# Optimization experiments

Hardware: AMD Instinct MI355X
Metric: run time of the kernel (lower is better)

## Reference

```python
import jax, jax.numpy as jnp
import numpy as np

H = 16  # num_heads

def setup_inputs() -> dict:
    key = jax.random.key(0)
    k1, k2, k3, k4 = jax.random.split(key, 4)
    B, N, E = 2, 2048, 2048
    return {
        "hidden_states": jax.random.normal(k1, (B, N, E), jnp.float32),
        "w_fused": jax.random.normal(k2, (E, 3 * E), jnp.float32) * (E ** -0.5),
        "w_proj": jax.random.normal(k3, (E, E), jnp.float32) * (E ** -0.5),
        "b_proj": jax.random.normal(k4, (E,), jnp.float32),
    }

def reference(hidden_states, w_fused, w_proj, b_proj):
    B, N, E = hidden_states.shape
    D = E // H  # head_dim
    qkv = hidden_states @ w_fused                      # [B,N,3E]
    q, k, v = jnp.split(qkv, 3, axis=-1)               # each [B,N,E]
    def to_heads(t):
        return t.reshape(B, N, H, D).transpose(0, 2, 1, 3)  # [B,H,N,D]
    q, k, v = to_heads(q), to_heads(k), to_heads(v)
    scores = jnp.einsum('bhnd,bhmd->bhnm', q, k) / jnp.asarray(D ** 0.5, q.dtype)
    causal = jnp.tril(jnp.ones((N, N), dtype=bool))    # [N,N]
    mask_value = jnp.asarray(jnp.finfo(scores.dtype).min, scores.dtype)
    scores = jnp.where(causal[None, None], scores, mask_value)
    attn_weights = jax.nn.softmax(scores, axis=-1)     # [B,H,N,N]
    attn_out = jnp.einsum('bhnm,bhmd->bhnd', attn_weights, v)
    attn_out = attn_out.transpose(0, 2, 1, 3).reshape(B, N, E)  # b n (h d)
    out = attn_out @ w_proj + b_proj
    return out, attn_weights
```

## Files before the change

### kernel.cpp

```cpp
#include <hip/hip_runtime.h>
#include <hip/hip_bf16.h>

typedef __attribute__((ext_vector_type(4))) float f32x4;
typedef __attribute__((ext_vector_type(8))) __bf16 bf16x8;


__device__ inline unsigned short f2bf(float f) {
  union { float f; unsigned u; } x; x.f = f;
  unsigned r = x.u + 0x7fffu + ((x.u >> 16) & 1u);
  return (unsigned short)(r >> 16);
}

__device__ inline void gload16(const ushort* g, ushort* l) {
  __builtin_amdgcn_global_load_lds(
      (const __attribute__((address_space(1))) unsigned int*)(const void*)g,
      (__attribute__((address_space(3))) unsigned int*)(void*)l, 16, 0, 0);
}

__device__ inline void stage64(const ushort* __restrict__ g, int ldg, ushort* l) {
  int tid = threadIdx.x;
#pragma unroll
  for (int t = 0; t < 4; ++t) {
    int c = tid + t * 256;
    int m = c >> 3, q = (c & 7) ^ (m & 7);
    gload16(g + (size_t)m * ldg + q * 8, l + c * 8);
  }
}

__device__ inline void stage_k64(const ushort* __restrict__ g, ushort* l) {
  int tid = threadIdx.x;
#pragma unroll
  for (int t = 0; t < 4; ++t) {
    int c = tid + t * 256;
    int m = c >> 4, q = (c & 15) ^ (m & 15);
    gload16(g + (size_t)m * 128 + q * 8, l + c * 8);
  }
}

__device__ inline void mma_tile64(const ushort* lA, const ushort* lB, f32x4 acc[4][4]) {
  int lane = threadIdx.x & 63, w = threadIdx.x >> 6;
  int wm = (w & 1) << 6, wn = (w >> 1) << 6;
  int row = lane & 15, quad = lane >> 4;
  int r7 = row & 7;
#pragma unroll
  for (int kk = 0; kk < 64; kk += 32) {
    int sw = (((kk >> 3) + quad) ^ r7) << 3;
    bf16x8 a[4], b[4];
#pragma unroll
    for (int i = 0; i < 4; ++i)
      a[i] = *(const bf16x8*)(lA + (wm + i * 16 + row) * 64 + sw);
#pragma unroll
    for (int j = 0; j < 4; ++j)
      b[j] = *(const bf16x8*)(lB + (wn + j * 16 + row) * 64 + sw);
#pragma unroll
    for (int i = 0; i < 4; ++i)
#pragma unroll
      for (int j = 0; j < 4; ++j)
        acc[i][j] = __builtin_amdgcn_mfma_f32_16x16x32_bf16(a[i], b[j], acc[i][j], 0, 0, 0);
  }
}


__global__ __launch_bounds__(256) void k_cvt_bf16(const float* __restrict__ in,
                                                  ushort* __restrict__ out, int n4) {
  int i = blockIdx.x * 256 + threadIdx.x;
  if (i >= n4) return;
  float4 v = *(const float4*)(in + (size_t)i * 4);
  ushort4 o; o.x = f2bf(v.x); o.y = f2bf(v.y); o.z = f2bf(v.z); o.w = f2bf(v.w);
  *(ushort4*)(out + (size_t)i * 4) = o;
}

__global__ __launch_bounds__(256) void k_transpose_bf16(const float* __restrict__ in,
                                                        ushort* __restrict__ out, int R, int C) {
  __shared__ __align__(16) ushort t[64][72];
  int c0 = blockIdx.x << 6, r0 = blockIdx.y << 6;
  int tid = threadIdx.x;
#pragma unroll
  for (int it = 0; it < 4; ++it) {
    int idx = tid + it * 256;
    int r = idx >> 4, c4 = (idx & 15) << 2;
    float4 v = *(const float4*)(in + (size_t)(r0 + r) * C + c0 + c4);
    t[c4][r] = f2bf(v.x); t[c4 + 1][r] = f2bf(v.y);
    t[c4 + 2][r] = f2bf(v.z); t[c4 + 3][r] = f2bf(v.w);
  }
  __syncthreads();
#pragma unroll
  for (int it = 0; it < 4; ++it) {
    int idx = tid + it * 256;
    int c = idx >> 4, r4 = (idx & 15) << 2;
    ushort4 o; o.x = t[c][r4]; o.y = t[c][r4 + 1]; o.z = t[c][r4 + 2]; o.w = t[c][r4 + 3];
    *(ushort4*)(out + (size_t)(c0 + c) * R + r0 + r4) = o;
  }
}

__global__ __launch_bounds__(256) void k_qkv(const ushort* __restrict__ A,
                                             const ushort* __restrict__ Bt,
                                             ushort* __restrict__ qh,
                                             ushort* __restrict__ kh,
                                             ushort* __restrict__ vt) {
  __shared__ __align__(16) ushort lA[128 * 64];
  __shared__ __align__(16) ushort lB[128 * 64];
  int rt = blockIdx.x, ct = blockIdx.y;
  f32x4 z = {0.f, 0.f, 0.f, 0.f};
  f32x4 acc[4][4];
#pragma unroll
  for (int i = 0; i < 4; ++i)
#pragma unroll
    for (int j = 0; j < 4; ++j) acc[i][j] = z;
  for (int kt = 0; kt < 2048; kt += 64) {
    __syncthreads();
    stage64(A + (size_t)rt * 128 * 2048 + kt, 2048, lA);
    stage64(Bt + (size_t)ct * 128 * 2048 + kt, 2048, lB);
    __syncthreads();
    mma_tile64(lA, lB, acc);
  }
  int lane = threadIdx.x & 63, w = threadIdx.x >> 6;
  int wm = (w & 1) << 6, wn = (w >> 1) << 6;
  int col = lane & 15, rb = (lane >> 4) << 2;
#pragma unroll
  for (int i = 0; i < 4; ++i)
#pragma unroll
    for (int j = 0; j < 4; ++j)
#pragma unroll
      for (int r = 0; r < 4; ++r) {
        int R = rt * 128 + wm + i * 16 + rb + r;
        int C = ct * 128 + wn + j * 16 + col;
        int b = R >> 11, n = R & 2047;
        int seg = C >> 11, hh = (C >> 7) & 15, d = C & 127;
        int bh = b * 16 + hh;
        float v = acc[i][j][r];
        if (seg == 0)      qh[((size_t)bh * 2048 + n) * 128 + d] = f2bf(v * 0.08838834764831845f);
        else if (seg == 1) kh[((size_t)bh * 2048 + n) * 128 + d] = f2bf(v);
        else               vt[((size_t)bh * 128 + d) * 2048 + n] = f2bf(v);
      }
}

__global__ __launch_bounds__(256, 4) void k_attn(const ushort* __restrict__ qh,
                                                 const ushort* __restrict__ kh,
                                                 const ushort* __restrict__ vt,
                                                 float* __restrict__ attnw,
                                                 ushort* __restrict__ Ao,
                                                 float* __restrict__ mf,
                                                 float* __restrict__ il) {
  __shared__ __align__(16) ushort lK[64 * 128];
  __shared__ __align__(16) ushort lV[128 * 64];
  __shared__ float mArr[64], lArr[64], corrArr[64], invA[64], tm0[64], tm1[64];

  int raw = blockIdx.x;
  int id = (raw & 7) * 128 + (raw >> 3);
  int t5 = id & 31, p = t5 >> 1;
  int rt = (t5 & 1) ? p : 31 - p;
  int bh = id >> 5;

  int tid = threadIdx.x;
  int lane = tid & 63, w = tid >> 6;
  int wm = (w & 1) << 5, wn = (w >> 1) << 5;
  int wpv = w << 5;
  int c16 = lane & 15, quad = lane >> 4;

  const ushort* Qb = qh + ((size_t)bh * 2048 + rt * 64) * 128;
  const ushort* Kb = kh + (size_t)bh * 2048 * 128;
  const ushort* Vb = vt + (size_t)bh * 128 * 2048;
  float* Pg = attnw + (size_t)bh * 2048 * 2048 + (size_t)(rt * 64) * 2048;

  bf16x8 q[2][4];
#pragma unroll
  for (int i = 0; i < 2; ++i)
#pragma unroll
    for (int ks = 0; ks < 4; ++ks)
      q[i][ks] = *(const bf16x8*)(Qb + (size_t)(wm + i * 16 + c16) * 128 + ks * 32 + quad * 8);

  if (tid < 64) { mArr[tid] = -INFINITY; lArr[tid] = 0.f; }

  f32x4 z = {0.f, 0.f, 0.f, 0.f};
  f32x4 o2[4][2];
#pragma unroll
  for (int i = 0; i < 4; ++i)
#pragma unroll
    for (int j = 0; j < 2; ++j) o2[i][j] = z;
  float* tmw = (wn == 0) ? tm0 : tm1;

  for (int ct = 0; ct <= rt; ++ct) {
    __syncthreads();
    stage_k64(Kb + (size_t)ct * 64 * 128, lK);
    __syncthreads();
    stage64(Vb + ct * 64, 2048, lV);

    f32x4 acc[2][2];
#pragma unroll
    for (int i = 0; i < 2; ++i)
#pragma unroll
      for (int j = 0; j < 2; ++j) acc[i][j] = z;
#pragma unroll
    for (int ks = 0; ks < 4; ++ks) {
      int sw = (((ks << 2) + quad) ^ c16) << 3;
      bf16x8 b[2];
#pragma unroll
      for (int j = 0; j < 2; ++j)
        b[j] = *(const bf16x8*)(lK + (wn + j * 16 + c16) * 128 + sw);
#pragma unroll
      for (int i = 0; i < 2; ++i)
#pragma unroll
        for (int j = 0; j < 2; ++j)
          acc[i][j] = __builtin_amdgcn_mfma_f32_16x16x32_bf16(q[i][ks], b[j], acc[i][j], 0, 0, 0);
    }

    bool diag = (ct == rt);
#pragma unroll
    for (int i = 0; i < 2; ++i)
#pragma unroll
      for (int r = 0; r < 4; ++r) {
        int lr = wm + i * 16 + quad * 4 + r;
        float mx = -INFINITY;
#pragma unroll
        for (int j = 0; j < 2; ++j) {
          int lc = wn + j * 16 + c16;
          if (!diag || lc <= lr) mx = fmaxf(mx, acc[i][j][r]);
        }
#pragma unroll
        for (int o = 1; o < 16; o <<= 1) mx = fmaxf(mx, __shfl_xor(mx, o));
        if (c16 == 0) tmw[lr] = mx;
      }
    __syncthreads();
    if (tid < 64) {
      float tmax = fmaxf(tm0[tid], tm1[tid]);
      float mo = mArr[tid];
      float mn = fmaxf(mo, tmax);
      float corr = (mo == -INFINITY) ? 0.f : __expf(mo - mn);
      mArr[tid] = mn; corrArr[tid] = corr; lArr[tid] *= corr;
    }
    __syncthreads();

#pragma unroll
    for (int i = 0; i < 2; ++i)
#pragma unroll
      for (int r = 0; r < 4; ++r) {
        int lr = wm + i * 16 + quad * 4 + r;
        float mn = mArr[lr];
        float s = 0.f;
        float* prow = Pg + (size_t)lr * 2048 + ct * 64;
#pragma unroll
        for (int j = 0; j < 2; ++j) {
          int lc = wn + j * 16 + c16;
          float sv = acc[i][j][r];
          prow[lc] = sv;
          float e = (!diag || lc <= lr) ? __expf(sv - mn) : 0.f;
          s += e;
          lK[lr * 64 + ((((lc >> 3) ^ (lr & 7)) << 3) | (lc & 7))] = f2bf(e);
        }
#pragma unroll
        for (int o = 1; o < 16; o <<= 1) s += __shfl_xor(s, o);
        if (c16 == 0) tmw[lr] = s;
      }
#pragma unroll
    for (int i = 0; i < 4; ++i)
#pragma unroll
      for (int r = 0; r < 4; ++r) {
        float cr = corrArr[i * 16 + quad * 4 + r];
#pragma unroll
        for (int j = 0; j < 2; ++j) o2[i][j][r] *= cr;
      }
    __syncthreads();
    if (tid < 64) lArr[tid] += tm0[tid] + tm1[tid];

#pragma unroll
    for (int ks = 0; ks < 2; ++ks) {
      int swp = (((ks << 2) + quad) ^ (c16 & 7)) << 3;
      bf16x8 a[4], b[2];
#pragma unroll
      for (int i = 0; i < 4; ++i)
        a[i] = *(const bf16x8*)(lK + (i * 16 + c16) * 64 + swp);
#pragma unroll
      for (int j = 0; j < 2; ++j)
        b[j] = *(const bf16x8*)(lV + (wpv + j * 16 + c16) * 64 + swp);
#pragma unroll
      for (int i = 0; i < 4; ++i)
#pragma unroll
        for (int j = 0; j < 2; ++j)
          o2[i][j] = __builtin_amdgcn_mfma_f32_16x16x32_bf16(a[i], b[j], o2[i][j], 0, 0, 0);
    }
  }

  if (tid < 64) {
    float iv = 1.f / lArr[tid];
    invA[tid] = iv;
    int g = bh * 2048 + rt * 64 + tid;
    mf[g] = mArr[tid]; il[g] = iv;
  }
  __syncthreads();
  int b_ = bh >> 4, hh = bh & 15;
#pragma unroll
  for (int i = 0; i < 4; ++i)
#pragma unroll
    for (int j = 0; j < 2; ++j)
#pragma unroll
      for (int r = 0; r < 4; ++r) {
        int row = i * 16 + quad * 4 + r;
        int col = wpv + j * 16 + c16;
        Ao[((size_t)b_ * 2048 + rt * 64 + row) * 2048 + hh * 128 + col] =
            f2bf(o2[i][j][r] * invA[row]);
      }
}

__global__ __launch_bounds__(256) void k_fixup(float* __restrict__ attnw,
                                               const float* __restrict__ mf,
                                               const float* __restrict__ il) {
  int n = blockIdx.x, bh = blockIdx.y;
  float m = mf[bh * 2048 + n];
  float inv = il[bh * 2048 + n];
  float* row = attnw + ((size_t)bh * 2048 + n) * 2048;
  int tid = threadIdx.x;
#pragma unroll
  for (int t = 0; t < 2; ++t) {
    int c0 = (tid + t * 256) << 2;
    float4 o;
    if (c0 + 3 <= n) {
      float4 s = *(const float4*)(row + c0);
      o.x = __expf(s.x - m) * inv; o.y = __expf(s.y - m) * inv;
      o.z = __expf(s.z - m) * inv; o.w = __expf(s.w - m) * inv;
    } else if (c0 > n) {
      o = make_float4(0.f, 0.f, 0.f, 0.f);
    } else {
      float4 s = *(const float4*)(row + c0);
      o.x = (c0     <= n) ? __expf(s.x - m) * inv : 0.f;
      o.y = (c0 + 1 <= n) ? __expf(s.y - m) * inv : 0.f;
      o.z = (c0 + 2 <= n) ? __expf(s.z - m) * inv : 0.f;
      o.w = (c0 + 3 <= n) ? __expf(s.w - m) * inv : 0.f;
    }
    *(float4*)(row + c0) = o;
  }
}

__global__ __launch_bounds__(256) void k_proj(const ushort* __restrict__ Ao,
                                              const ushort* __restrict__ Wt,
                                              const float* __restrict__ bias,
                                              float* __restrict__ out) {
  int rt = blockIdx.x, ct = blockIdx.y;
  __shared__ __align__(16) ushort lA[128 * 64];
  __shared__ __align__(16) ushort lB[128 * 64];
  f32x4 z = {0.f, 0.f, 0.f, 0.f};
  f32x4 acc[4][4];
#pragma unroll
  for (int i = 0; i < 4; ++i)
#pragma unroll
    for (int j = 0; j < 4; ++j) acc[i][j] = z;
  for (int kt = 0; kt < 2048; kt += 64) {
    __syncthreads();
    stage64(Ao + (size_t)rt * 128 * 2048 + kt, 2048, lA);
    stage64(Wt + (size_t)ct * 128 * 2048 + kt, 2048, lB);
    __syncthreads();
    mma_tile64(lA, lB, acc);
  }
  int lane = threadIdx.x & 63, w = threadIdx.x >> 6;
  int wm = (w & 1) << 6, wn = (w >> 1) << 6;
  int col = lane & 15, rb = (lane >> 4) << 2;
#pragma unroll
  for (int i = 0; i < 4; ++i)
#pragma unroll
    for (int j = 0; j < 4; ++j)
#pragma unroll
      for (int r = 0; r < 4; ++r) {
        int R = rt * 128 + wm + i * 16 + rb + r;
        int C = ct * 128 + wn + j * 16 + col;
        out[(size_t)R * 2048 + C] = acc[i][j][r] + bias[C];
      }
}


extern "C" void kernel_launch(void* const* d_in, const int* in_sizes, int n_in,
                              void* d_out, int out_size, void* d_ws, size_t ws_size,
                              hipStream_t stream) {
  const float* hs = (const float*)d_in[0];
  const float* wf = (const float*)d_in[1];
  const float* wp = (const float*)d_in[2];
  const float* bp = (const float*)d_in[3];
  float* out = (float*)d_out;
  float* attnw = out + (size_t)8388608;

  ushort* Hb  = (ushort*)d_ws;
  ushort* Wft = Hb  + (size_t)8388608;
  ushort* Wpt = Wft + (size_t)12582912;
  ushort* qh  = Wpt + (size_t)4194304;
  ushort* kh  = qh  + (size_t)8388608;
  ushort* vt  = kh  + (size_t)8388608;
  ushort* Ao  = vt  + (size_t)8388608;
  float* mf = (float*)Hb;
  float* il = mf + 65536;

  k_cvt_bf16<<<8192, 256, 0, stream>>>(hs, Hb, 2097152);
  k_transpose_bf16<<<dim3(96, 32), 256, 0, stream>>>(wf, Wft, 2048, 6144);
  k_transpose_bf16<<<dim3(32, 32), 256, 0, stream>>>(wp, Wpt, 2048, 2048);
  k_qkv<<<dim3(32, 48), 256, 0, stream>>>(Hb, Wft, qh, kh, vt);
  k_attn<<<1024, 256, 0, stream>>>(qh, kh, vt, attnw, Ao, mf, il);
  k_fixup<<<dim3(2048, 32), 256, 0, stream>>>(attnw, mf, il);
  k_proj<<<dim3(32, 16), 256, 0, stream>>>(Ao, Wpt, bp, out);
}
```

Before: 1.156 ms.

## Fuse softmax fixup pass into attention kernel tail and raise MFMA priority

Removes the separate k_fixup launch. Each attention block now rescales its own 64 rows of raw scores (exp(s-m)*inv and causal zeroing) at the end of the kernel, using the max and inverse sum it already holds in shared memory, so the mf/il workspace round trip goes away. It also wraps both MFMA loops in s_setprio(1)/s_setprio(0) to favour matrix issue across waves. Trade-off: the fixup pass now runs serially in each block's tail, and the raw rows may still be in cache, but the work imbalance of causal blocks now extends into this full-row pass.

```diff
diff --git a/kernel.cpp b/kernel.cpp
--- a/kernel.cpp
+++ b/kernel.cpp
@@ -139,9 +139,7 @@
                                                  const ushort* __restrict__ kh,
                                                  const ushort* __restrict__ vt,
                                                  float* __restrict__ attnw,
-                                                 ushort* __restrict__ Ao,
-                                                 float* __restrict__ mf,
-                                                 float* __restrict__ il) {
+                                                 ushort* __restrict__ Ao) {
   __shared__ __align__(16) ushort lK[64 * 128];
   __shared__ __align__(16) ushort lV[128 * 64];
   __shared__ float mArr[64], lArr[64], corrArr[64], invA[64], tm0[64], tm1[64];
@@ -191,6 +189,7 @@
     for (int i = 0; i < 2; ++i)
 #pragma unroll
       for (int j = 0; j < 2; ++j) acc[i][j] = z;
+    __builtin_amdgcn_s_setprio(1);
 #pragma unroll
     for (int ks = 0; ks < 4; ++ks) {
       int sw = (((ks << 2) + quad) ^ c16) << 3;
@@ -204,6 +203,7 @@
         for (int j = 0; j < 2; ++j)
           acc[i][j] = __builtin_amdgcn_mfma_f32_16x16x32_bf16(q[i][ks], b[j], acc[i][j], 0, 0, 0);
     }
+    __builtin_amdgcn_s_setprio(0);
 
     bool diag = (ct == rt);
 #pragma unroll
@@ -263,6 +263,7 @@
     __syncthreads();
     if (tid < 64) lArr[tid] += tm0[tid] + tm1[tid];
 
+    __builtin_amdgcn_s_setprio(1);
 #pragma unroll
     for (int ks = 0; ks < 2; ++ks) {
       int swp = (((ks << 2) + quad) ^ (c16 & 7)) << 3;
@@ -279,14 +280,10 @@
         for (int j = 0; j < 2; ++j)
           o2[i][j] = __builtin_amdgcn_mfma_f32_16x16x32_bf16(a[i], b[j], o2[i][j], 0, 0, 0);
     }
-  }
-
-  if (tid < 64) {
-    float iv = 1.f / lArr[tid];
-    invA[tid] = iv;
-    int g = bh * 2048 + rt * 64 + tid;
-    mf[g] = mArr[tid]; il[g] = iv;
-  }
+    __builtin_amdgcn_s_setprio(0);
+  }
+
+  if (tid < 64) invA[tid] = 1.f / lArr[tid];
   __syncthreads();
   int b_ = bh >> 4, hh = bh & 15;
 #pragma unroll
@@ -300,19 +297,14 @@
         Ao[((size_t)b_ * 2048 + rt * 64 + row) * 2048 + hh * 128 + col] =
             f2bf(o2[i][j][r] * invA[row]);
       }
-}
-
-__global__ __launch_bounds__(256) void k_fixup(float* __restrict__ attnw,
-                                               const float* __restrict__ mf,
-                                               const float* __restrict__ il) {
-  int n = blockIdx.x, bh = blockIdx.y;
-  float m = mf[bh * 2048 + n];
-  float inv = il[bh * 2048 + n];
-  float* row = attnw + ((size_t)bh * 2048 + n) * 2048;
-  int tid = threadIdx.x;
-#pragma unroll
-  for (int t = 0; t < 2; ++t) {
-    int c0 = (tid + t * 256) << 2;
+
+  for (int it = 0; it < 128; ++it) {
+    int idx = tid + it * 256;
+    int r = idx >> 9;
+    int c0 = (idx & 511) << 2;
+    int n = rt * 64 + r;
+    float m = mArr[r], inv = invA[r];
+    float* row = Pg + (size_t)r * 2048;
     float4 o;
     if (c0 + 3 <= n) {
       float4 s = *(const float4*)(row + c0);
@@ -384,14 +376,11 @@
   ushort* kh  = qh  + (size_t)8388608;
   ushort* vt  = kh  + (size_t)8388608;
   ushort* Ao  = vt  + (size_t)8388608;
-  float* mf = (float*)Hb;
-  float* il = mf + 65536;
 
   k_cvt_bf16<<<8192, 256, 0, stream>>>(hs, Hb, 2097152);
   k_transpose_bf16<<<dim3(96, 32), 256, 0, stream>>>(wf, Wft, 2048, 6144);
   k_transpose_bf16<<<dim3(32, 32), 256, 0, stream>>>(wp, Wpt, 2048, 2048);
   k_qkv<<<dim3(32, 48), 256, 0, stream>>>(Hb, Wft, qh, kh, vt);
-  k_attn<<<1024, 256, 0, stream>>>(qh, kh, vt, attnw, Ao, mf, il);
-  k_fixup<<<dim3(2048, 32), 256, 0, stream>>>(attnw, mf, il);
+  k_attn<<<1024, 256, 0, stream>>>(qh, kh, vt, attnw, Ao);
   k_proj<<<dim3(32, 16), 256, 0, stream>>>(Ao, Wpt, bp, out);
 }
```

After: 1.230 ms. 6.4% more time.

## Give each wave full row ownership in attention to drop cross-wave softmax syncs

Applied to the files above, without the earlier changes.

Splits the attention tile so each of the four waves owns 16 whole query rows across all 64 key columns and the full 128-wide head dim. Softmax max and sum now stay in registers with only intra-wave shuffles, which removes the shared-memory row-stat arrays and most per-iteration __syncthreads. P gets its own LDS buffer instead of reusing lK, so K and V can be staged behind a single barrier, and s_setprio is raised around the MFMA sections. In exchange each wave holds more accumulators and loads more B fragments, so register pressure rises.

```diff
diff --git a/kernel.cpp b/kernel.cpp
--- a/kernel.cpp
+++ b/kernel.cpp
@@ -144,7 +144,7 @@
                                                  float* __restrict__ il) {
   __shared__ __align__(16) ushort lK[64 * 128];
   __shared__ __align__(16) ushort lV[128 * 64];
-  __shared__ float mArr[64], lArr[64], corrArr[64], invA[64], tm0[64], tm1[64];
+  __shared__ __align__(16) ushort lP[64 * 64];
 
   int raw = blockIdx.x;
   int id = (raw & 7) * 128 + (raw >> 3);
@@ -154,152 +154,120 @@
 
   int tid = threadIdx.x;
   int lane = tid & 63, w = tid >> 6;
-  int wm = (w & 1) << 5, wn = (w >> 1) << 5;
-  int wpv = w << 5;
   int c16 = lane & 15, quad = lane >> 4;
+  int wr = w << 4;
 
   const ushort* Qb = qh + ((size_t)bh * 2048 + rt * 64) * 128;
   const ushort* Kb = kh + (size_t)bh * 2048 * 128;
   const ushort* Vb = vt + (size_t)bh * 128 * 2048;
   float* Pg = attnw + (size_t)bh * 2048 * 2048 + (size_t)(rt * 64) * 2048;
 
-  bf16x8 q[2][4];
-#pragma unroll
-  for (int i = 0; i < 2; ++i)
-#pragma unroll
-    for (int ks = 0; ks < 4; ++ks)
-      q[i][ks] = *(const bf16x8*)(Qb + (size_t)(wm + i * 16 + c16) * 128 + ks * 32 + quad * 8);
-
-  if (tid < 64) { mArr[tid] = -INFINITY; lArr[tid] = 0.f; }
+  bf16x8 q[4];
+#pragma unroll
+  for (int ks = 0; ks < 4; ++ks)
+    q[ks] = *(const bf16x8*)(Qb + (size_t)(wr + c16) * 128 + ks * 32 + quad * 8);
+
+  float m_[4], l_[4];
+#pragma unroll
+  for (int r = 0; r < 4; ++r) { m_[r] = -INFINITY; l_[r] = 0.f; }
 
   f32x4 z = {0.f, 0.f, 0.f, 0.f};
-  f32x4 o2[4][2];
-#pragma unroll
-  for (int i = 0; i < 4; ++i)
-#pragma unroll
-    for (int j = 0; j < 2; ++j) o2[i][j] = z;
-  float* tmw = (wn == 0) ? tm0 : tm1;
+  f32x4 o2[8];
+#pragma unroll
+  for (int j = 0; j < 8; ++j) o2[j] = z;
 
   for (int ct = 0; ct <= rt; ++ct) {
     __syncthreads();
     stage_k64(Kb + (size_t)ct * 64 * 128, lK);
-    __syncthreads();
     stage64(Vb + ct * 64, 2048, lV);
-
-    f32x4 acc[2][2];
-#pragma unroll
-    for (int i = 0; i < 2; ++i)
-#pragma unroll
-      for (int j = 0; j < 2; ++j) acc[i][j] = z;
+    __syncthreads();
+
+    f32x4 acc[4];
+#pragma unroll
+    for (int j = 0; j < 4; ++j) acc[j] = z;
+    __builtin_amdgcn_s_setprio(1);
 #pragma unroll
     for (int ks = 0; ks < 4; ++ks) {
       int sw = (((ks << 2) + quad) ^ c16) << 3;
-      bf16x8 b[2];
-#pragma unroll
-      for (int j = 0; j < 2; ++j)
-        b[j] = *(const bf16x8*)(lK + (wn + j * 16 + c16) * 128 + sw);
-#pragma unroll
-      for (int i = 0; i < 2; ++i)
-#pragma unroll
-        for (int j = 0; j < 2; ++j)
-          acc[i][j] = __builtin_amdgcn_mfma_f32_16x16x32_bf16(q[i][ks], b[j], acc[i][j], 0, 0, 0);
-    }
+      bf16x8 b[4];
+#pragma unroll
+      for (int j = 0; j < 4; ++j)
+        b[j] = *(const bf16x8*)(lK + (j * 16 + c16) * 128 + sw);
+#pragma unroll
+      for (int j = 0; j < 4; ++j)
+        acc[j] = __builtin_amdgcn_mfma_f32_16x16x32_bf16(q[ks], b[j], acc[j], 0, 0, 0);
+    }
+    __builtin_amdgcn_s_setprio(0);
 
     bool diag = (ct == rt);
 #pragma unroll
-    for (int i = 0; i < 2; ++i)
-#pragma unroll
-      for (int r = 0; r < 4; ++r) {
-        int lr = wm + i * 16 + quad * 4 + r;
-        float mx = -INFINITY;
-#pragma unroll
-        for (int j = 0; j < 2; ++j) {
-          int lc = wn + j * 16 + c16;
-          if (!diag || lc <= lr) mx = fmaxf(mx, acc[i][j][r]);
-        }
-#pragma unroll
-        for (int o = 1; o < 16; o <<= 1) mx = fmaxf(mx, __shfl_xor(mx, o));
-        if (c16 == 0) tmw[lr] = mx;
+    for (int r = 0; r < 4; ++r) {
+      int lr = wr + quad * 4 + r;
+      float mx = -INFINITY;
+#pragma unroll
+      for (int j = 0; j < 4; ++j) {
+        int lc = j * 16 + c16;
+        if (!diag || lc <= lr) mx = fmaxf(mx, acc[j][r]);
       }
-    __syncthreads();
-    if (tid < 64) {
-      float tmax = fmaxf(tm0[tid], tm1[tid]);
-      float mo = mArr[tid];
-      float mn = fmaxf(mo, tmax);
-      float corr = (mo == -INFINITY) ? 0.f : __expf(mo - mn);
-      mArr[tid] = mn; corrArr[tid] = corr; lArr[tid] *= corr;
-    }
-    __syncthreads();
-
-#pragma unroll
-    for (int i = 0; i < 2; ++i)
-#pragma unroll
-      for (int r = 0; r < 4; ++r) {
-        int lr = wm + i * 16 + quad * 4 + r;
-        float mn = mArr[lr];
-        float s = 0.f;
-        float* prow = Pg + (size_t)lr * 2048 + ct * 64;
-#pragma unroll
-        for (int j = 0; j < 2; ++j) {
-          int lc = wn + j * 16 + c16;
-          float sv = acc[i][j][r];
-          prow[lc] = sv;
-          float e = (!diag || lc <= lr) ? __expf(sv - mn) : 0.f;
-          s += e;
-          lK[lr * 64 + ((((lc >> 3) ^ (lr & 7)) << 3) | (lc & 7))] = f2bf(e);
-        }
-#pragma unroll
-        for (int o = 1; o < 16; o <<= 1) s += __shfl_xor(s, o);
-        if (c16 == 0) tmw[lr] = s;
+#pragma unroll
+      for (int o = 1; o < 16; o <<= 1) mx = fmaxf(mx, __shfl_xor(mx, o));
+      float mn = fmaxf(m_[r], mx);
+      float corr = (m_[r] == -INFINITY) ? 0.f : __expf(m_[r] - mn);
+      float s = 0.f;
+      float* prow = Pg + (size_t)lr * 2048 + ct * 64;
+#pragma unroll
+      for (int j = 0; j < 4; ++j) {
+        int lc = j * 16 + c16;
+        float sv = acc[j][r];
+        prow[lc] = sv;
+        float e = (!diag || lc <= lr) ? __expf(sv - mn) : 0.f;
+        s += e;
+        lP[lr * 64 + ((((lc >> 3) ^ (lr & 7)) << 3) | (lc & 7))] = f2bf(e);
       }
 #pragma unroll
-    for (int i = 0; i < 4; ++i)
-#pragma unroll
-      for (int r = 0; r < 4; ++r) {
-        float cr = corrArr[i * 16 + quad * 4 + r];
-#pragma unroll
-        for (int j = 0; j < 2; ++j) o2[i][j][r] *= cr;
-      }
-    __syncthreads();
-    if (tid < 64) lArr[tid] += tm0[tid] + tm1[tid];
-
+      for (int o = 1; o < 16; o <<= 1) s += __shfl_xor(s, o);
+      m_[r] = mn;
+      l_[r] = l_[r] * corr + s;
+#pragma unroll
+      for (int j = 0; j < 8; ++j) o2[j][r] *= corr;
+    }
+
+    __builtin_amdgcn_s_setprio(1);
 #pragma unroll
     for (int ks = 0; ks < 2; ++ks) {
       int swp = (((ks << 2) + quad) ^ (c16 & 7)) << 3;
-      bf16x8 a[4], b[2];
-#pragma unroll
-      for (int i = 0; i < 4; ++i)
-        a[i] = *(const bf16x8*)(lK + (i * 16 + c16) * 64 + swp);
-#pragma unroll
-      for (int j = 0; j < 2; ++j)
-        b[j] = *(const bf16x8*)(lV + (wpv + j * 16 + c16) * 64 + swp);
-#pragma unroll
-      for (int i = 0; i < 4; ++i)
-#pragma unroll
-        for (int j = 0; j < 2; ++j)
-          o2[i][j] = __builtin_amdgcn_mfma_f32_16x16x32_bf16(a[i], b[j], o2[i][j], 0, 0, 0);
-    }
-  }
-
-  if (tid < 64) {
-    float iv = 1.f / lArr[tid];
-    invA[tid] = iv;
-    int g = bh * 2048 + rt * 64 + tid;
-    mf[g] = mArr[tid]; il[g] = iv;
-  }
-  __syncthreads();
+      bf16x8 a = *(const bf16x8*)(lP + (wr + c16) * 64 + swp);
+      bf16x8 b[8];
+#pragma unroll
+      for (int j = 0; j < 8; ++j)
+        b[j] = *(const bf16x8*)(lV + (j * 16 + c16) * 64 + swp);
+#pragma unroll
+      for (int j = 0; j < 8; ++j)
+        o2[j] = __builtin_amdgcn_mfma_f32_16x16x32_bf16(a, b[j], o2[j], 0, 0, 0);
+    }
+    __builtin_amdgcn_s_setprio(0);
+  }
+
+  float inv_[4];
+#pragma unroll
+  for (int r = 0; r < 4; ++r) inv_[r] = 1.f / l_[r];
+  if (c16 == 0) {
+#pragma unroll
+    for (int r = 0; r < 4; ++r) {
+      int g = bh * 2048 + rt * 64 + wr + quad * 4 + r;
+      mf[g] = m_[r]; il[g] = inv_[r];
+    }
+  }
   int b_ = bh >> 4, hh = bh & 15;
 #pragma unroll
-  for (int i = 0; i < 4; ++i)
-#pragma unroll
-    for (int j = 0; j < 2; ++j)
-#pragma unroll
-      for (int r = 0; r < 4; ++r) {
-        int row = i * 16 + quad * 4 + r;
-        int col = wpv + j * 16 + c16;
-        Ao[((size_t)b_ * 2048 + rt * 64 + row) * 2048 + hh * 128 + col] =
-            f2bf(o2[i][j][r] * invA[row]);
-      }
+  for (int j = 0; j < 8; ++j)
+#pragma unroll
+    for (int r = 0; r < 4; ++r) {
+      int row = wr + quad * 4 + r;
+      int col = j * 16 + c16;
+      Ao[((size_t)b_ * 2048 + rt * 64 + row) * 2048 + hh * 128 + col] =
+          f2bf(o2[j][r] * inv_[r]);
+    }
 }
 
 __global__ __launch_bounds__(256) void k_fixup(float* __restrict__ attnw,
```

Result: faster. 1.068 ms (-7.6%).
